# Performance work log

Measured on AMD Instinct MI355X. Metric: run time of the kernel, lower is better.

Reference implementation:

```python
import jax, jax.numpy as jnp
import numpy as np

D_MODEL = 1024
N_HEADS = 16
HEAD_DIM = D_MODEL // N_HEADS  # 64
WINDOW = 64
HALF = WINDOW // 2  # query i attends keys in [i-HALF, i+HALF]
CHUNK = WINDOW      # chunk size for banded attention; must be >= HALF and divide S
B, S = 4, 4096


def setup_inputs() -> dict:
    key = jax.random.key(0)
    ks = jax.random.split(key, 6)
    s = 0.02
    D = D_MODEL
    return {
        "x":  jax.random.normal(ks[0], (B, S, D), jnp.float32),
        "Wq": jax.random.normal(ks[1], (D, D), jnp.float32) * s,
        "bq": jnp.zeros((D,), jnp.float32),
        "Wk": jax.random.normal(ks[2], (D, D), jnp.float32) * s,
        "bk": jnp.zeros((D,), jnp.float32),
        "Wv": jax.random.normal(ks[3], (D, D), jnp.float32) * s,
        "bv": jnp.zeros((D,), jnp.float32),
        "Wo": jax.random.normal(ks[4], (D, D), jnp.float32) * s,
        "bo": jnp.zeros((D,), jnp.float32),
    }


def reference(x, Wq, bq, Wk, bk, Wv, bv, Wo, bo):
    # Sliding-window attention (seq_len > 128 path of SparseAttention).
    b, s, d = x.shape
    h, hd = N_HEADS, HEAD_DIM
    scale = 1.0 / np.sqrt(hd).astype(np.float32)

    q = (x @ Wq.T + bq).reshape(b, s, h, hd)
    k = (x @ Wk.T + bk).reshape(b, s, h, hd)
    v = (x @ Wv.T + bv).reshape(b, s, h, hd)

    c = CHUNK
    nb = s // c
    qc = q.reshape(b, nb, c, h, hd)

    # Pad one chunk of zeros on each side; each query chunk attends keys in
    # chunks [n-1, n, n+1] (covers the +/-HALF band since HALF <= c).
    pad = jnp.zeros((b, c, h, hd), q.dtype)
    kp = jnp.concatenate([pad, k, pad], axis=1).reshape(b, nb + 2, c, h, hd)
    vp = jnp.concatenate([pad, v, pad], axis=1).reshape(b, nb + 2, c, h, hd)
    k3 = jnp.concatenate([kp[:, :-2], kp[:, 1:-1], kp[:, 2:]], axis=2)  # [b,nb,3c,h,hd]
    v3 = jnp.concatenate([vp[:, :-2], vp[:, 1:-1], vp[:, 2:]], axis=2)

    # scores: [b,h,nb,c,3c]
    scores = jnp.einsum('bnqhd,bnkhd->bhnqk', qc, k3) * scale

    # Banded validity mask. Global query pos = n*c + i ; global key pos = n*c + j - c.
    i = jnp.arange(c)[:, None]          # [c,1]
    j = jnp.arange(3 * c)[None, :]      # [1,3c]
    rel = j - c - i                     # key_pos - query_pos, [c,3c]
    band = (rel >= -HALF) & (rel <= HALF)
    n = jnp.arange(nb)[:, None, None]   # [nb,1,1]
    keypos = n * c + (j - c)[None, :, :]  # [nb,1,3c]
    valid = band[None, :, :] & (keypos >= 0) & (keypos < s)  # [nb,c,3c]

    attn = jax.nn.softmax(jnp.where(valid[None, None], scores, -jnp.inf), axis=-1)
    ctx = jnp.einsum('bhnqk,bnkhd->bnqhd', attn, v3).reshape(b, s, d)
    return ctx @ Wo.T + bo
```

## Files before the change

kernel.cpp:

```cpp
#include <hip/hip_runtime.h>
#include <hip/hip_bf16.h>
#include <cstdint>
#include <cstddef>

#define D_MODEL 1024
#define NHEADS  16
#define HDIM    64
#define HALFW   32
#define BATCH   4
#define SEQ     4096
#define MROWS   (BATCH*SEQ)

typedef __attribute__((ext_vector_type(8))) short        bf16x8;
typedef __attribute__((ext_vector_type(4))) float        f32x4;
typedef __attribute__((ext_vector_type(4))) unsigned int u32x4;

typedef const __attribute__((address_space(1))) void gvoid_t;
typedef __attribute__((address_space(3))) void       lvoid_t;

__device__ __forceinline__ unsigned short f2bf(float f) {
    unsigned int u = __float_as_uint(f);
    u += 0x7fffu + ((u >> 16) & 1u);
    return (unsigned short)(u >> 16);
}

__device__ __forceinline__ int vswz(int row, int bytecol) {
    return (row * 256 + bytecol) ^ (((row ^ (row >> 3)) & 7) << 4);
}

__global__ __launch_bounds__(256)
void cvt_f32_bf16(const float* __restrict__ src, unsigned short* __restrict__ dst, int n8) {
    int i = blockIdx.x * 256 + threadIdx.x;
    if (i >= n8) return;
    float4 a = *(const float4*)(src + (size_t)i * 8);
    float4 b = *(const float4*)(src + (size_t)i * 8 + 4);
    u32x4 o;
    o[0] = (unsigned)f2bf(a.x) | ((unsigned)f2bf(a.y) << 16);
    o[1] = (unsigned)f2bf(a.z) | ((unsigned)f2bf(a.w) << 16);
    o[2] = (unsigned)f2bf(b.x) | ((unsigned)f2bf(b.y) << 16);
    o[3] = (unsigned)f2bf(b.z) | ((unsigned)f2bf(b.w) << 16);
    *(u32x4*)(dst + (size_t)i * 8) = o;
}

__global__ __launch_bounds__(256)
void cvt4_f32_bf16(const float* __restrict__ s0, const float* __restrict__ s1,
                   const float* __restrict__ s2, const float* __restrict__ s3,
                   unsigned short* __restrict__ d0, unsigned short* __restrict__ d1,
                   unsigned short* __restrict__ d2, unsigned short* __restrict__ d3, int n8) {
    int i = blockIdx.x * 256 + threadIdx.x;
    if (i >= n8) return;
    const float* src = blockIdx.y == 0 ? s0 : blockIdx.y == 1 ? s1 : blockIdx.y == 2 ? s2 : s3;
    unsigned short* dst = blockIdx.y == 0 ? d0 : blockIdx.y == 1 ? d1 : blockIdx.y == 2 ? d2 : d3;
    float4 a = *(const float4*)(src + (size_t)i * 8);
    float4 b = *(const float4*)(src + (size_t)i * 8 + 4);
    u32x4 o;
    o[0] = (unsigned)f2bf(a.x) | ((unsigned)f2bf(a.y) << 16);
    o[1] = (unsigned)f2bf(a.z) | ((unsigned)f2bf(a.w) << 16);
    o[2] = (unsigned)f2bf(b.x) | ((unsigned)f2bf(b.y) << 16);
    o[3] = (unsigned)f2bf(b.z) | ((unsigned)f2bf(b.w) << 16);
    *(u32x4*)(dst + (size_t)i * 8) = o;
}

template <int NOUT, int F32OUT>
__global__ __launch_bounds__(512)
void gemm256(const unsigned short* __restrict__ A,
             const unsigned short* __restrict__ W0,
             const unsigned short* __restrict__ W1,
             const unsigned short* __restrict__ W2,
             const float* __restrict__ b0, const float* __restrict__ b1,
             const float* __restrict__ b2,
             unsigned short* __restrict__ o0, unsigned short* __restrict__ o1,
             unsigned short* __restrict__ o2, float* __restrict__ of32)
{
    constexpr int K  = 1024;
    constexpr int HT = K / 32;
    constexpr int NWG = 64 * 4 * NOUT;
    __shared__ unsigned short lds[65536];

    const int tid  = threadIdx.x;
    const int wave = tid >> 6, lane = tid & 63;
    const int wr = wave >> 2, wc = wave & 3;

    const int bid = blockIdx.x;
    const int g   = (bid & 7) * (NWG / 8) + (bid >> 3);
    const int rb  = g / (4 * NOUT);
    const int cb  = g % (4 * NOUT);
    const int which = cb >> 2;
    const int bm = rb * 256, bn = (cb & 3) * 256;

    const unsigned short* W = (NOUT == 1 || which == 0) ? W0 : (which == 1 ? W1 : W2);
    const float* bias       = (NOUT == 1 || which == 0) ? b0 : (which == 1 ? b1 : b2);
    unsigned short* obf     = (NOUT == 1 || which == 0) ? o0 : (which == 1 ? o1 : o2);

    f32x4 acc[8][4];
    #pragma unroll
    for (int m = 0; m < 8; ++m)
        #pragma unroll
        for (int n = 0; n < 4; ++n)
            #pragma unroll
            for (int j = 0; j < 4; ++j) acc[m][n][j] = 0.0f;

    char* ldsb = (char*)lds;

    const int idx0 = tid, idx1 = tid + 512;
    const int r0 = idx0 >> 2, r1 = idx1 >> 2;
    const int c0 = ((idx0 & 3) - (r0 >> 1)) & 3;
    const int c1 = ((idx1 & 3) - (r1 >> 1)) & 3;
    const size_t sA0 = (size_t)(bm + r0) * K + c0 * 8;
    const size_t sA1 = (size_t)(bm + r1) * K + c1 * 8;
    const size_t sB0 = (size_t)(bn + r0) * K + c0 * 8;
    const size_t sB1 = (size_t)(bn + r1) * K + c1 * 8;
    const int ldsW = wave * 1024;

    auto STAGE = [&](int h, int isA) {
        const int base = (isA ? 0 : 65536) + (h & 3) * 16384 + ldsW;
        const int ke = h * 32;
        const unsigned short* M = isA ? A : W;
        const size_t s0 = isA ? sA0 : sB0;
        const size_t s1 = isA ? sA1 : sB1;
        __builtin_amdgcn_global_load_lds((gvoid_t*)(M + s0 + ke),
            (lvoid_t*)(ldsb + base), 16, 0, 0);
        __builtin_amdgcn_global_load_lds((gvoid_t*)(M + s1 + ke),
            (lvoid_t*)(ldsb + base + 8192), 16, 0, 0);
    };

    const int lr = lane & 15;
    const int pp = (((lane >> 4) + (lr >> 1)) & 3) << 4;
    const int abase = (wr * 128 + lr) * 64 + pp;
    const int bbase = 65536 + (wc * 64 + lr) * 64 + pp;

    STAGE(0, 1); STAGE(0, 0); STAGE(1, 1); STAGE(1, 0); STAGE(2, 1); STAGE(2, 0);
    asm volatile("s_waitcnt vmcnt(8)" ::: "memory");
    __builtin_amdgcn_s_barrier();

    #pragma unroll 1
    for (int hp = 0; hp < HT; ++hp) {
        const int so = (hp & 3) * 16384;
        bf16x8 aL[4], bb[4], aH[4];
        #pragma unroll
        for (int m = 0; m < 4; ++m) aL[m] = *(const bf16x8*)(ldsb + so + abase + m * 1024);
        #pragma unroll
        for (int n = 0; n < 4; ++n) bb[n] = *(const bf16x8*)(ldsb + so + bbase + n * 1024);
        __builtin_amdgcn_sched_barrier(0);
        if (hp + 3 < HT) STAGE(hp + 3, 1);
        __builtin_amdgcn_sched_barrier(0);
        __builtin_amdgcn_s_barrier();
        asm volatile("s_waitcnt lgkmcnt(0)" ::: "memory");
        __builtin_amdgcn_sched_barrier(0);
        __builtin_amdgcn_s_setprio(1);
        #pragma unroll
        for (int m = 0; m < 4; ++m)
            #pragma unroll
            for (int n = 0; n < 4; ++n)
                acc[m][n] = __builtin_amdgcn_mfma_f32_16x16x32_bf16(aL[m], bb[n], acc[m][n], 0, 0, 0);
        __builtin_amdgcn_s_setprio(0);
        __builtin_amdgcn_sched_barrier(0);
        __builtin_amdgcn_s_barrier();
        #pragma unroll
        for (int m = 0; m < 4; ++m) aH[m] = *(const bf16x8*)(ldsb + so + abase + (m + 4) * 1024);
        __builtin_amdgcn_sched_barrier(0);
        if (hp + 3 < HT) STAGE(hp + 3, 0);
        if (hp <= HT - 4)      { asm volatile("s_waitcnt vmcnt(8)" ::: "memory"); }
        else if (hp == HT - 3) { asm volatile("s_waitcnt vmcnt(4)" ::: "memory"); }
        else if (hp == HT - 2) { asm volatile("s_waitcnt vmcnt(0)" ::: "memory"); }
        __builtin_amdgcn_sched_barrier(0);
        __builtin_amdgcn_s_barrier();
        asm volatile("s_waitcnt lgkmcnt(0)" ::: "memory");
        __builtin_amdgcn_sched_barrier(0);
        __builtin_amdgcn_s_setprio(1);
        #pragma unroll
        for (int m = 0; m < 4; ++m)
            #pragma unroll
            for (int n = 0; n < 4; ++n)
                acc[m + 4][n] = __builtin_amdgcn_mfma_f32_16x16x32_bf16(aH[m], bb[n], acc[m + 4][n], 0, 0, 0);
        __builtin_amdgcn_s_setprio(0);
        __builtin_amdgcn_sched_barrier(0);
        __builtin_amdgcn_s_barrier();
    }

    float bvv[4];
    #pragma unroll
    for (int n = 0; n < 4; ++n) bvv[n] = bias[bn + wc * 64 + n * 16 + lr];
    #pragma unroll
    for (int m = 0; m < 8; ++m) {
        #pragma unroll
        for (int j = 0; j < 4; ++j) {
            const int row = bm + wr * 128 + m * 16 + (lane >> 4) * 4 + j;
            #pragma unroll
            for (int n = 0; n < 4; ++n) {
                const int col = bn + wc * 64 + n * 16 + lr;
                const float v = acc[m][n][j] + bvv[n];
                if (F32OUT) of32[(size_t)row * 1024 + col] = v;
                else        obf[(size_t)row * 1024 + col]  = f2bf(v);
            }
        }
    }
}

__global__ __launch_bounds__(256)
void attn_band(const unsigned short* __restrict__ Q,
               const unsigned short* __restrict__ Kk,
               const unsigned short* __restrict__ V,
               unsigned short* __restrict__ Ctx)
{
    __shared__ unsigned short Qs[64 * 72];
    __shared__ unsigned short Ks[128 * 72];
    __shared__ unsigned short Vt[64 * 128];
    __shared__ unsigned short Ps[64 * 128];

    const int qt = blockIdx.x, h = blockIdx.y, b = blockIdx.z;
    const int qbase  = qt * 64;
    const int kstart = qbase - HALFW;
    const int tid = threadIdx.x, wave = tid >> 6, lane = tid & 63;

    const size_t base = (size_t)b * SEQ * D_MODEL + (size_t)h * HDIM;
    const unsigned short* Qb = Q  + base;
    const unsigned short* Kb = Kk + base;
    const unsigned short* Vb = V  + base;
    unsigned short*       Cb = Ctx + base;

    for (int c = tid; c < 512; c += 256) {
        const int row = c >> 3, col = (c & 7) * 8;
        *(u32x4*)(Qs + row * 72 + col) =
            *(const u32x4*)(Qb + (size_t)(qbase + row) * D_MODEL + col);
    }
    for (int c = tid; c < 1024; c += 256) {
        const int krow = c >> 3, col = (c & 7) * 8;
        const int kpos = kstart + krow;
        u32x4 kv;
        if (kpos >= 0 && kpos < SEQ) {
            kv = *(const u32x4*)(Kb + (size_t)kpos * D_MODEL + col);
        } else {
            for (int j = 0; j < 4; ++j) kv[j] = 0u;
        }
        *(u32x4*)(Ks + krow * 72 + col) = kv;
    }
    for (int c = tid; c < 512; c += 256) {
        const int p = c >> 3, dch = c & 7;
        const int k0 = kstart + 2 * p, k1 = k0 + 1;
        u32x4 v0, v1;
        if (k0 >= 0 && k0 < SEQ) {
            v0 = *(const u32x4*)(Vb + (size_t)k0 * D_MODEL + dch * 8);
        } else {
            for (int j = 0; j < 4; ++j) v0[j] = 0u;
        }
        if (k1 >= 0 && k1 < SEQ) {
            v1 = *(const u32x4*)(Vb + (size_t)k1 * D_MODEL + dch * 8);
        } else {
            for (int j = 0; j < 4; ++j) v1[j] = 0u;
        }
        #pragma unroll
        for (int j = 0; j < 8; ++j) {
            const int d = dch * 8 + j;
            const unsigned lo = (v0[j >> 1] >> ((j & 1) * 16)) & 0xffffu;
            const unsigned hi = (v1[j >> 1] >> ((j & 1) * 16)) & 0xffffu;
            *(unsigned*)((char*)Vt + vswz(d, 4 * p)) = lo | (hi << 16);
        }
    }
    __syncthreads();

    f32x4 sc[8];
    #pragma unroll
    for (int c = 0; c < 8; ++c)
        #pragma unroll
        for (int j = 0; j < 4; ++j) sc[c][j] = 0.0f;

    bf16x8 aq[2];
    #pragma unroll
    for (int kc = 0; kc < 2; ++kc)
        aq[kc] = *(const bf16x8*)(Qs + (wave * 16 + (lane & 15)) * 72 + kc * 32 + (lane >> 4) * 8);
    #pragma unroll
    for (int c = 0; c < 8; ++c) {
        #pragma unroll
        for (int kc = 0; kc < 2; ++kc) {
            bf16x8 bk_ = *(const bf16x8*)(Ks + (c * 16 + (lane & 15)) * 72 + kc * 32 + (lane >> 4) * 8);
            sc[c] = __builtin_amdgcn_mfma_f32_16x16x32_bf16(aq[kc], bk_, sc[c], 0, 0, 0);
        }
    }

    const int grp = lane >> 4, colk = lane & 15;
    float rowmax[4] = {-1e30f, -1e30f, -1e30f, -1e30f};
    #pragma unroll
    for (int c = 0; c < 8; ++c) {
        const int kpos = kstart + c * 16 + colk;
        #pragma unroll
        for (int j = 0; j < 4; ++j) {
            const int qpos = qbase + wave * 16 + grp * 4 + j;
            const int rel = kpos - qpos;
            const bool valid = (kpos >= 0) && (kpos < SEQ) && (rel >= -HALFW) && (rel <= HALFW);
            const float v = valid ? sc[c][j] * 0.125f : -1e30f;
            sc[c][j] = v;
            rowmax[j] = fmaxf(rowmax[j], v);
        }
    }
    #pragma unroll
    for (int j = 0; j < 4; ++j)
        #pragma unroll
        for (int m = 1; m < 16; m <<= 1)
            rowmax[j] = fmaxf(rowmax[j], __shfl_xor(rowmax[j], m, 64));

    float rowsum[4] = {0.f, 0.f, 0.f, 0.f};
    #pragma unroll
    for (int c = 0; c < 8; ++c)
        #pragma unroll
        for (int j = 0; j < 4; ++j) {
            const float p = __expf(sc[c][j] - rowmax[j]);
            sc[c][j] = p;
            rowsum[j] += p;
        }
    #pragma unroll
    for (int j = 0; j < 4; ++j)
        #pragma unroll
        for (int m = 1; m < 16; m <<= 1)
            rowsum[j] += __shfl_xor(rowsum[j], m, 64);

    #pragma unroll
    for (int c = 0; c < 8; ++c)
        #pragma unroll
        for (int j = 0; j < 4; ++j)
            *(unsigned short*)((char*)Ps + vswz(wave * 16 + grp * 4 + j, (c * 16 + colk) * 2))
                = f2bf(sc[c][j]);
    __syncthreads();

    f32x4 o[4];
    #pragma unroll
    for (int n = 0; n < 4; ++n)
        #pragma unroll
        for (int j = 0; j < 4; ++j) o[n][j] = 0.0f;
    #pragma unroll
    for (int kc = 0; kc < 4; ++kc) {
        bf16x8 pa = *(const bf16x8*)((const char*)Ps +
                        vswz(wave * 16 + (lane & 15), kc * 64 + (lane >> 4) * 16));
        #pragma unroll
        for (int n = 0; n < 4; ++n) {
            bf16x8 bv_ = *(const bf16x8*)((const char*)Vt +
                            vswz(n * 16 + (lane & 15), kc * 64 + (lane >> 4) * 16));
            o[n] = __builtin_amdgcn_mfma_f32_16x16x32_bf16(pa, bv_, o[n], 0, 0, 0);
        }
    }

    float rinv[4];
    #pragma unroll
    for (int j = 0; j < 4; ++j) rinv[j] = 1.0f / rowsum[j];
    #pragma unroll
    for (int n = 0; n < 4; ++n)
        #pragma unroll
        for (int j = 0; j < 4; ++j) {
            const int q = qbase + wave * 16 + grp * 4 + j;
            Cb[(size_t)q * D_MODEL + n * 16 + colk] = f2bf(o[n][j] * rinv[j]);
        }
}

extern "C" void kernel_launch(void* const* d_in, const int* in_sizes, int n_in,
                              void* d_out, int out_size, void* d_ws, size_t ws_size,
                              hipStream_t stream)
{
    (void)in_sizes; (void)n_in; (void)out_size; (void)ws_size;
    const float* x  = (const float*)d_in[0];
    const float* Wq = (const float*)d_in[1];
    const float* bq = (const float*)d_in[2];
    const float* Wk = (const float*)d_in[3];
    const float* bk = (const float*)d_in[4];
    const float* Wv = (const float*)d_in[5];
    const float* bv = (const float*)d_in[6];
    const float* Wo = (const float*)d_in[7];
    const float* bo = (const float*)d_in[8];
    float* out = (float*)d_out;

    char* ws = (char*)d_ws;
    unsigned short* xb  = (unsigned short*)ws;
    unsigned short* wqb = (unsigned short*)(ws + 33554432);
    unsigned short* wkb = wqb + 1048576;
    unsigned short* wvb = wkb + 1048576;
    unsigned short* wob = wvb + 1048576;
    unsigned short* qb  = wob + 1048576;
    unsigned short* kb  = qb + (size_t)MROWS * D_MODEL;
    unsigned short* vb  = kb + (size_t)MROWS * D_MODEL;
    unsigned short* ctxb = xb;

    cvt_f32_bf16<<<dim3(MROWS * D_MODEL / 8 / 256), 256, 0, stream>>>(x, xb, MROWS * D_MODEL / 8);
    cvt4_f32_bf16<<<dim3(D_MODEL * D_MODEL / 8 / 256, 4), 256, 0, stream>>>(
        Wq, Wk, Wv, Wo, wqb, wkb, wvb, wob, D_MODEL * D_MODEL / 8);

    gemm256<3, 0><<<dim3(768), 512, 0, stream>>>(
        xb, wqb, wkb, wvb, bq, bk, bv, qb, kb, vb, nullptr);

    attn_band<<<dim3(SEQ / 64, NHEADS, BATCH), 256, 0, stream>>>(qb, kb, vb, ctxb);

    gemm256<1, 1><<<dim3(256), 512, 0, stream>>>(
        ctxb, wob, wob, wob, bo, bo, bo, nullptr, nullptr, nullptr, out);
}
```

Baseline: 238.1 us.

## Ping-pong GEMM main loop between wave groups so loads and MFMAs alternate

Restructures the GEMM K-loop into a ping-pong schedule. One half of the waves (wr==0) reads LDS fragments while the other half issues MFMAs, and the roles swap each phase, with the lagging group finishing one iteration late. Each K-step now uses one full 8x4 MFMA block instead of two half-blocks, and both global-to-LDS stages are issued together. The aim is to overlap LDS reads with matrix-core work across waves. The cost is more fragment registers held live and a different barrier structure that relies on the lagging group's reads finishing before the next stage overwrites the buffer.

```diff
diff --git a/kernel.cpp b/kernel.cpp
--- a/kernel.cpp
+++ b/kernel.cpp
@@ -80,6 +80,7 @@
     const int tid  = threadIdx.x;
     const int wave = tid >> 6, lane = tid & 63;
     const int wr = wave >> 2, wc = wave & 3;
+    const bool isX = (wr == 0);
 
     const int bid = blockIdx.x;
     const int g   = (bid & 7) * (NWG / 8) + (bid >> 3);
@@ -133,49 +134,61 @@
     asm volatile("s_waitcnt vmcnt(8)" ::: "memory");
     __builtin_amdgcn_s_barrier();
 
+    bf16x8 fa[8], fb[4];
+
     #pragma unroll 1
     for (int hp = 0; hp < HT; ++hp) {
         const int so = (hp & 3) * 16384;
-        bf16x8 aL[4], bb[4], aH[4];
-        #pragma unroll
-        for (int m = 0; m < 4; ++m) aL[m] = *(const bf16x8*)(ldsb + so + abase + m * 1024);
-        #pragma unroll
-        for (int n = 0; n < 4; ++n) bb[n] = *(const bf16x8*)(ldsb + so + bbase + n * 1024);
-        __builtin_amdgcn_sched_barrier(0);
-        if (hp + 3 < HT) STAGE(hp + 3, 1);
+        if (isX) {
+            #pragma unroll
+            for (int m = 0; m < 8; ++m) fa[m] = *(const bf16x8*)(ldsb + so + abase + m * 1024);
+            #pragma unroll
+            for (int n = 0; n < 4; ++n) fb[n] = *(const bf16x8*)(ldsb + so + bbase + n * 1024);
+        } else if (hp > 0) {
+            asm volatile("s_waitcnt lgkmcnt(0)" ::: "memory");
+            __builtin_amdgcn_sched_barrier(0);
+            __builtin_amdgcn_s_setprio(1);
+            #pragma unroll
+            for (int m = 0; m < 8; ++m)
+                #pragma unroll
+                for (int n = 0; n < 4; ++n)
+                    acc[m][n] = __builtin_amdgcn_mfma_f32_16x16x32_bf16(fa[m], fb[n], acc[m][n], 0, 0, 0);
+            __builtin_amdgcn_s_setprio(0);
+        }
         __builtin_amdgcn_sched_barrier(0);
         __builtin_amdgcn_s_barrier();
+        if (hp + 3 < HT) { STAGE(hp + 3, 1); STAGE(hp + 3, 0); }
+        __builtin_amdgcn_sched_barrier(0);
+        if (isX) {
+            asm volatile("s_waitcnt lgkmcnt(0)" ::: "memory");
+            __builtin_amdgcn_sched_barrier(0);
+            __builtin_amdgcn_s_setprio(1);
+            #pragma unroll
+            for (int m = 0; m < 8; ++m)
+                #pragma unroll
+                for (int n = 0; n < 4; ++n)
+                    acc[m][n] = __builtin_amdgcn_mfma_f32_16x16x32_bf16(fa[m], fb[n], acc[m][n], 0, 0, 0);
+            __builtin_amdgcn_s_setprio(0);
+        } else {
+            #pragma unroll
+            for (int m = 0; m < 8; ++m) fa[m] = *(const bf16x8*)(ldsb + so + abase + m * 1024);
+            #pragma unroll
+            for (int n = 0; n < 4; ++n) fb[n] = *(const bf16x8*)(ldsb + so + bbase + n * 1024);
+        }
+        __builtin_amdgcn_sched_barrier(0);
+        if (hp <= HT - 4)      { asm volatile("s_waitcnt vmcnt(8)" ::: "memory"); }
+        else if (hp == HT - 3) { asm volatile("s_waitcnt vmcnt(4)" ::: "memory"); }
+        else                   { asm volatile("s_waitcnt vmcnt(0)" ::: "memory"); }
+        __builtin_amdgcn_s_barrier();
+    }
+    if (!isX) {
         asm volatile("s_waitcnt lgkmcnt(0)" ::: "memory");
         __builtin_amdgcn_sched_barrier(0);
-        __builtin_amdgcn_s_setprio(1);
-        #pragma unroll
-        for (int m = 0; m < 4; ++m)
+        #pragma unroll
+        for (int m = 0; m < 8; ++m)
             #pragma unroll
             for (int n = 0; n < 4; ++n)
-                acc[m][n] = __builtin_amdgcn_mfma_f32_16x16x32_bf16(aL[m], bb[n], acc[m][n], 0, 0, 0);
-        __builtin_amdgcn_s_setprio(0);
-        __builtin_amdgcn_sched_barrier(0);
-        __builtin_amdgcn_s_barrier();
-        #pragma unroll
-        for (int m = 0; m < 4; ++m) aH[m] = *(const bf16x8*)(ldsb + so + abase + (m + 4) * 1024);
-        __builtin_amdgcn_sched_barrier(0);
-        if (hp + 3 < HT) STAGE(hp + 3, 0);
-        if (hp <= HT - 4)      { asm volatile("s_waitcnt vmcnt(8)" ::: "memory"); }
-        else if (hp == HT - 3) { asm volatile("s_waitcnt vmcnt(4)" ::: "memory"); }
-        else if (hp == HT - 2) { asm volatile("s_waitcnt vmcnt(0)" ::: "memory"); }
-        __builtin_amdgcn_sched_barrier(0);
-        __builtin_amdgcn_s_barrier();
-        asm volatile("s_waitcnt lgkmcnt(0)" ::: "memory");
-        __builtin_amdgcn_sched_barrier(0);
-        __builtin_amdgcn_s_setprio(1);
-        #pragma unroll
-        for (int m = 0; m < 4; ++m)
-            #pragma unroll
-            for (int n = 0; n < 4; ++n)
-                acc[m + 4][n] = __builtin_amdgcn_mfma_f32_16x16x32_bf16(aH[m], bb[n], acc[m + 4][n], 0, 0, 0);
-        __builtin_amdgcn_s_setprio(0);
-        __builtin_amdgcn_sched_barrier(0);
-        __builtin_amdgcn_s_barrier();
+                acc[m][n] = __builtin_amdgcn_mfma_f32_16x16x32_bf16(fa[m], fb[n], acc[m][n], 0, 0, 0);
     }
 
     float bvv[4];
```

After: 231.4 us. 2.8% less time.

## Replace 256x256 GEMM with 256x128 double-buffered tile at two blocks per CU

Applied to the files above, without the earlier changes.

Replaces the 512-thread 256x256-tile GEMM, which used a hand-scheduled 4-stage LDS ring with split MFMA phases and explicit waitcnts, with a 256-thread 256x128-tile kernel. The new kernel uses a simple two-slot double buffer, 48KB of LDS per block, and launch bounds allowing two blocks per CU. The aim is higher occupancy and more blocks (1536 and 512) to fill the GPU, hiding latency through concurrent blocks instead of manual scheduling. In exchange it gives up the deeper prefetch, priority hints and interleaving, and reloads A twice as often per output.

```diff
diff --git a/kernel.cpp b/kernel.cpp
--- a/kernel.cpp
+++ b/kernel.cpp
@@ -62,8 +62,8 @@
 }
 
 template <int NOUT, int F32OUT>
-__global__ __launch_bounds__(512)
-void gemm256(const unsigned short* __restrict__ A,
+__global__ __launch_bounds__(256, 2)
+void gemm_db(const unsigned short* __restrict__ A,
              const unsigned short* __restrict__ W0,
              const unsigned short* __restrict__ W1,
              const unsigned short* __restrict__ W2,
@@ -74,19 +74,19 @@
 {
     constexpr int K  = 1024;
     constexpr int HT = K / 32;
-    constexpr int NWG = 64 * 4 * NOUT;
-    __shared__ unsigned short lds[65536];
+    constexpr int CBG = 8 * NOUT;
+    __shared__ unsigned short lds[2 * 12288];
 
     const int tid  = threadIdx.x;
     const int wave = tid >> 6, lane = tid & 63;
-    const int wr = wave >> 2, wc = wave & 3;
+    const int wr = wave >> 1, wc = wave & 1;
 
     const int bid = blockIdx.x;
-    const int g   = (bid & 7) * (NWG / 8) + (bid >> 3);
-    const int rb  = g / (4 * NOUT);
-    const int cb  = g % (4 * NOUT);
-    const int which = cb >> 2;
-    const int bm = rb * 256, bn = (cb & 3) * 256;
+    const int g   = (bid & 7) * (8 * CBG) + (bid >> 3);
+    const int rb  = g / CBG;
+    const int cbg = g % CBG;
+    const int which = cbg >> 3;
+    const int bm = rb * 256, bn = (cbg & 7) * 128;
 
     const unsigned short* W = (NOUT == 1 || which == 0) ? W0 : (which == 1 ? W1 : W2);
     const float* bias       = (NOUT == 1 || which == 0) ? b0 : (which == 1 ? b1 : b2);
@@ -102,80 +102,52 @@
 
     char* ldsb = (char*)lds;
 
-    const int idx0 = tid, idx1 = tid + 512;
-    const int r0 = idx0 >> 2, r1 = idx1 >> 2;
-    const int c0 = ((idx0 & 3) - (r0 >> 1)) & 3;
-    const int c1 = ((idx1 & 3) - (r1 >> 1)) & 3;
-    const size_t sA0 = (size_t)(bm + r0) * K + c0 * 8;
-    const size_t sA1 = (size_t)(bm + r1) * K + c1 * 8;
-    const size_t sB0 = (size_t)(bn + r0) * K + c0 * 8;
-    const size_t sB1 = (size_t)(bn + r1) * K + c1 * 8;
+    const int ra  = tid >> 2;
+    const int ks  = ((tid & 3) - (ra >> 1)) & 3;
+    const size_t sA[4] = { (size_t)(bm + ra) * K + ks * 8,
+                           (size_t)(bm + ra + 64)  * K + ks * 8,
+                           (size_t)(bm + ra + 128) * K + ks * 8,
+                           (size_t)(bm + ra + 192) * K + ks * 8 };
+    const size_t sB[2] = { (size_t)(bn + ra) * K + ks * 8,
+                           (size_t)(bn + ra + 64)  * K + ks * 8 };
     const int ldsW = wave * 1024;
 
-    auto STAGE = [&](int h, int isA) {
-        const int base = (isA ? 0 : 65536) + (h & 3) * 16384 + ldsW;
+    auto STAGE = [&](int h) {
+        const int slot = (h & 1) * 24576;
         const int ke = h * 32;
-        const unsigned short* M = isA ? A : W;
-        const size_t s0 = isA ? sA0 : sB0;
-        const size_t s1 = isA ? sA1 : sB1;
-        __builtin_amdgcn_global_load_lds((gvoid_t*)(M + s0 + ke),
-            (lvoid_t*)(ldsb + base), 16, 0, 0);
-        __builtin_amdgcn_global_load_lds((gvoid_t*)(M + s1 + ke),
-            (lvoid_t*)(ldsb + base + 8192), 16, 0, 0);
+        #pragma unroll
+        for (int i = 0; i < 4; ++i)
+            __builtin_amdgcn_global_load_lds((gvoid_t*)(A + sA[i] + ke),
+                (lvoid_t*)(ldsb + slot + ldsW + i * 4096), 16, 0, 0);
+        #pragma unroll
+        for (int i = 0; i < 2; ++i)
+            __builtin_amdgcn_global_load_lds((gvoid_t*)(W + sB[i] + ke),
+                (lvoid_t*)(ldsb + slot + 16384 + ldsW + i * 4096), 16, 0, 0);
     };
 
     const int lr = lane & 15;
     const int pp = (((lane >> 4) + (lr >> 1)) & 3) << 4;
     const int abase = (wr * 128 + lr) * 64 + pp;
-    const int bbase = 65536 + (wc * 64 + lr) * 64 + pp;
-
-    STAGE(0, 1); STAGE(0, 0); STAGE(1, 1); STAGE(1, 0); STAGE(2, 1); STAGE(2, 0);
-    asm volatile("s_waitcnt vmcnt(8)" ::: "memory");
-    __builtin_amdgcn_s_barrier();
+    const int bbase = 16384 + (wc * 64 + lr) * 64 + pp;
+
+    STAGE(0);
+    __syncthreads();
 
     #pragma unroll 1
-    for (int hp = 0; hp < HT; ++hp) {
-        const int so = (hp & 3) * 16384;
-        bf16x8 aL[4], bb[4], aH[4];
-        #pragma unroll
-        for (int m = 0; m < 4; ++m) aL[m] = *(const bf16x8*)(ldsb + so + abase + m * 1024);
-        #pragma unroll
-        for (int n = 0; n < 4; ++n) bb[n] = *(const bf16x8*)(ldsb + so + bbase + n * 1024);
-        __builtin_amdgcn_sched_barrier(0);
-        if (hp + 3 < HT) STAGE(hp + 3, 1);
-        __builtin_amdgcn_sched_barrier(0);
-        __builtin_amdgcn_s_barrier();
-        asm volatile("s_waitcnt lgkmcnt(0)" ::: "memory");
-        __builtin_amdgcn_sched_barrier(0);
-        __builtin_amdgcn_s_setprio(1);
-        #pragma unroll
-        for (int m = 0; m < 4; ++m)
+    for (int h = 0; h < HT; ++h) {
+        const char* sl = ldsb + (h & 1) * 24576;
+        if (h + 1 < HT) STAGE(h + 1);
+        bf16x8 fa[8], fb[4];
+        #pragma unroll
+        for (int m = 0; m < 8; ++m) fa[m] = *(const bf16x8*)(sl + abase + m * 1024);
+        #pragma unroll
+        for (int n = 0; n < 4; ++n) fb[n] = *(const bf16x8*)(sl + bbase + n * 1024);
+        #pragma unroll
+        for (int m = 0; m < 8; ++m)
             #pragma unroll
             for (int n = 0; n < 4; ++n)
-                acc[m][n] = __builtin_amdgcn_mfma_f32_16x16x32_bf16(aL[m], bb[n], acc[m][n], 0, 0, 0);
-        __builtin_amdgcn_s_setprio(0);
-        __builtin_amdgcn_sched_barrier(0);
-        __builtin_amdgcn_s_barrier();
-        #pragma unroll
-        for (int m = 0; m < 4; ++m) aH[m] = *(const bf16x8*)(ldsb + so + abase + (m + 4) * 1024);
-        __builtin_amdgcn_sched_barrier(0);
-        if (hp + 3 < HT) STAGE(hp + 3, 0);
-        if (hp <= HT - 4)      { asm volatile("s_waitcnt vmcnt(8)" ::: "memory"); }
-        else if (hp == HT - 3) { asm volatile("s_waitcnt vmcnt(4)" ::: "memory"); }
-        else if (hp == HT - 2) { asm volatile("s_waitcnt vmcnt(0)" ::: "memory"); }
-        __builtin_amdgcn_sched_barrier(0);
-        __builtin_amdgcn_s_barrier();
-        asm volatile("s_waitcnt lgkmcnt(0)" ::: "memory");
-        __builtin_amdgcn_sched_barrier(0);
-        __builtin_amdgcn_s_setprio(1);
-        #pragma unroll
-        for (int m = 0; m < 4; ++m)
-            #pragma unroll
-            for (int n = 0; n < 4; ++n)
-                acc[m + 4][n] = __builtin_amdgcn_mfma_f32_16x16x32_bf16(aH[m], bb[n], acc[m + 4][n], 0, 0, 0);
-        __builtin_amdgcn_s_setprio(0);
-        __builtin_amdgcn_sched_barrier(0);
-        __builtin_amdgcn_s_barrier();
+                acc[m][n] = __builtin_amdgcn_mfma_f32_16x16x32_bf16(fa[m], fb[n], acc[m][n], 0, 0, 0);
+        __syncthreads();
     }
 
     float bvv[4];
@@ -382,11 +354,11 @@
     cvt4_f32_bf16<<<dim3(D_MODEL * D_MODEL / 8 / 256, 4), 256, 0, stream>>>(
         Wq, Wk, Wv, Wo, wqb, wkb, wvb, wob, D_MODEL * D_MODEL / 8);
 
-    gemm256<3, 0><<<dim3(768), 512, 0, stream>>>(
+    gemm_db<3, 0><<<dim3(1536), 256, 0, stream>>>(
         xb, wqb, wkb, wvb, bq, bk, bv, qb, kb, vb, nullptr);
 
     attn_band<<<dim3(SEQ / 64, NHEADS, BATCH), 256, 0, stream>>>(qb, kb, vb, ctxb);
 
-    gemm256<1, 1><<<dim3(256), 512, 0, stream>>>(
+    gemm_db<1, 1><<<dim3(512), 256, 0, stream>>>(
         ctxb, wob, wob, wob, bo, bo, bo, nullptr, nullptr, nullptr, out);
 }
```

New measurement: 232.5 us. 1.02x faster.
